# Kernel optimization log

Hardware: AMD Instinct MI355X
Metric: run time of the kernel (lower is better)

## Reference

```python
import jax, jax.numpy as jnp
import numpy as np
from jax.scipy.linalg import expm, solve_triangular

B, N, K, A, V = 2, 256, 16, 16, 32000
ALPHA = 1.0
LAMBDA_BELIEF = 1.0
EPS = 1e-8   # kl_divergence jitter
EPS2 = 1e-6  # pairwise-KL jitter


def _spd(key, b, n, k, scale=0.3):
    a = jax.random.normal(key, (b, n, k, k)) * scale
    return jnp.einsum('bnkl,bnml->bnkm', a, a) + jnp.eye(k)


def setup_inputs() -> dict:
    key = jax.random.key(0)
    ks = jax.random.split(key, 9)
    mu = jax.random.normal(ks[0], (B, N, K))
    Sigma = _spd(ks[1], B, N, K)
    phi = jax.random.normal(ks[2], (B, N, A)) * 0.05
    mu_prior = jax.random.normal(ks[3], (B, N, K))
    Sigma_prior = _spd(ks[4], B, N, K)
    beta = jax.random.uniform(ks[5], (B, N, N)) / N
    W_out = jax.random.normal(ks[6], (V, K)) * 0.02
    R = jax.random.normal(ks[7], (A, K, K))
    generators = (R - jnp.swapaxes(R, -1, -2)) * 0.1  # skew-symmetric Lie generators
    targets = jax.random.randint(ks[8], (B, N), 0, V)
    return {"mu": mu, "Sigma": Sigma, "phi": phi, "mu_prior": mu_prior,
            "Sigma_prior": Sigma_prior, "beta": beta, "W_out": W_out,
            "generators": generators, "targets": targets}


def _bexpm(M):
    # batched matrix exponential over leading dims
    shape = M.shape
    return jax.vmap(expm)(M.reshape(-1, shape[-2], shape[-1])).reshape(shape)


def _potential(mu, Sigma, phi, mu_prior, Sigma_prior, beta, W_out, generators, targets):
    I = jnp.eye(K, dtype=mu.dtype)

    # --- V_self: alpha * sum_n KL(q_n || p_n), explicit-inverse formulation ---
    Sq = Sigma + EPS * I
    Sp = Sigma_prior + EPS * I
    Sp_inv = jnp.linalg.inv(Sp)
    trace_t = jnp.einsum('bnij,bnji->bn', Sp_inv, Sq)
    dmu = mu_prior - mu
    mahal = jnp.einsum('bni,bnij,bnj->bn', dmu, Sp_inv, dmu)
    logdet = jnp.linalg.slogdet(Sp)[1] - jnp.linalg.slogdet(Sq)[1]
    kl_self = 0.5 * (trace_t + mahal - K + logdet)
    V_self = ALPHA * kl_self.sum(-1)

    # --- V_align: pairwise KL under Lie transport Omega_ij = e^{phi_i G} e^{-phi_j G} ---
    phi_mat = jnp.einsum('bna,aij->bnij', phi, generators)          # (B,N,K,K)
    exp_phi = _bexpm(phi_mat)
    exp_neg_phi = _bexpm(-phi_mat)
    Omega = jnp.einsum('bikl,bjlm->bijkm', exp_phi, exp_neg_phi)    # (B,N,N,K,K)
    mu_t = jnp.einsum('bijkl,bjl->bijk', Omega, mu)                 # (B,N,N,K)
    # Omega Sigma_j Omega^T (congruence -> SPD)
    Sigma_t = jnp.einsum('bijkl,bjlm,bijnm->bijkn', Omega, Sigma, Omega)

    Stp = Sigma_t + EPS2 * I
    L_p = jnp.linalg.cholesky(Stp)                                  # (B,N,N,K,K)
    Sigma_i = jnp.broadcast_to((Sigma + EPS2 * I)[:, :, None], (B, N, N, K, K))
    Y = solve_triangular(L_p, Sigma_i, lower=True)
    Z = solve_triangular(jnp.swapaxes(L_p, -1, -2), Y, lower=False)
    trace_term = jnp.diagonal(Z, axis1=-2, axis2=-1).sum(-1)        # (B,N,N)

    delta = mu_t - mu[:, :, None, :]
    v = solve_triangular(L_p, delta[..., None], lower=True)[..., 0]
    mahal_term = (v ** 2).sum(-1)

    logdet_p = 2.0 * jnp.log(jnp.diagonal(L_p, axis1=-2, axis2=-1) + EPS2).sum(-1)
    L_q = jnp.linalg.cholesky(Sigma + EPS2 * I)                     # (B,N,K,K)
    logdet_q = 2.0 * jnp.log(jnp.diagonal(L_q, axis1=-2, axis2=-1) + EPS2).sum(-1)

    kl_all = 0.5 * (trace_term + mahal_term - K + logdet_p - logdet_q[:, :, None])
    kl_all = jnp.maximum(kl_all, 0.0)
    kl_all = kl_all * (1.0 - jnp.eye(N, dtype=mu.dtype))            # zero diagonal
    V_align = LAMBDA_BELIEF * (beta * kl_all).sum((-2, -1))

    # --- V_ce: cross entropy over W_out projection of mu ---
    logits = jnp.einsum('bnk,vk->bnv', mu, W_out)
    logp = jax.nn.log_softmax(logits, axis=-1)
    ce = -jnp.take_along_axis(logp, targets[..., None], axis=-1)[..., 0]
    V_ce = ce.sum(-1)

    return V_self + V_align + V_ce


def reference(mu, Sigma, phi, mu_prior, Sigma_prior, beta, W_out, generators, targets):
    return _potential(mu, Sigma, phi, mu_prior, Sigma_prior, beta, W_out, generators, targets)
```

## Files before the change

kernel.cpp:

```cpp
#include <hip/hip_runtime.h>
#include <math.h>

#define NB 2
#define NN 256
#define KD 16
#define VV 32000
#define EPS_SELF 1e-8f
#define EPS_AL   1e-6f
#define NNODES (NB*NN)

#define CE_ROWS 8
#define CE_CH   32
#define CE_CHUNK (VV/CE_CH)

#define OFF_MT  0
#define OFF_SH  (NNODES*16)
#define OFF_P   (OFF_SH + NNODES*256)
#define OFF_LD  (OFF_P + NNODES*256)
#define OFF_KLS (OFF_LD + NNODES)
#define OFF_CE  (OFF_KLS + NNODES)
#define OFF_AP  (OFF_CE + NNODES)
#define OFF_CEP (OFF_AP + NNODES)
#define WS_FLOATS (OFF_CEP + NNODES*CE_CH)

__device__ inline float blockReduceSum256(float v, float* red) {
  #pragma unroll
  for (int o = 32; o; o >>= 1) v += __shfl_down(v, o);
  __syncthreads();
  if ((threadIdx.x & 63) == 0) red[threadIdx.x >> 6] = v;
  __syncthreads();
  float s = red[0] + red[1] + red[2] + red[3];
  __syncthreads();
  return s;
}

__global__ __launch_bounds__(256) void prep_kernel(
    const float* __restrict__ mu, const float* __restrict__ Sigma,
    const float* __restrict__ phi, const float* __restrict__ mu_prior,
    const float* __restrict__ Sigma_prior, const float* __restrict__ gen,
    float* __restrict__ ws)
{
  __shared__ float bufA[256], bufT[256], bufU[256], bufS[256];
  __shared__ float srow[16], scol[16], vec_s[16], phi_s[16], red[4];
  const int tid = threadIdx.x;
  const int r = tid >> 4, c = tid & 15;
  const int bid = blockIdx.x;
  const int role = bid & 1, node = bid >> 1;

  if (role == 0) {
    if (tid < 16) phi_s[tid] = phi[node*16 + tid];
    bufS[tid] = Sigma[node*256 + tid];
    __syncthreads();
    float pm = 0.f;
    #pragma unroll
    for (int a = 0; a < 16; ++a) pm = fmaf(phi_s[a], gen[a*256 + tid], pm);
    bufA[tid] = pm * 0.125f;
    __syncthreads();
    float Mrow[16];
    #pragma unroll
    for (int j = 0; j < 16; ++j) Mrow[j] = bufA[r*16 + j];
    bufT[tid] = ((r == c) ? 1.f : 0.f) + bufA[tid] * 0.125f;
    __syncthreads();
    for (int k = 7; k >= 1; --k) {
      float acc = 0.f;
      #pragma unroll
      for (int j = 0; j < 16; ++j) acc = fmaf(Mrow[j], bufT[j*16 + c], acc);
      __syncthreads();
      bufT[tid] = ((r == c) ? 1.f : 0.f) + acc / (float)k;
      __syncthreads();
    }
    for (int s = 0; s < 3; ++s) {
      float acc = 0.f;
      #pragma unroll
      for (int j = 0; j < 16; ++j) acc = fmaf(bufT[r*16 + j], bufT[j*16 + c], acc);
      __syncthreads();
      bufT[tid] = acc;
      __syncthreads();
    }
    {
      float acc = 0.f;
      #pragma unroll
      for (int j = 0; j < 16; ++j) acc = fmaf(bufS[r*16 + j], bufT[j*16 + c], acc);
      bufU[tid] = acc;
    }
    __syncthreads();
    {
      float sh = 0.f;
      #pragma unroll
      for (int j = 0; j < 16; ++j) sh = fmaf(bufT[j*16 + r], bufU[j*16 + c], sh);
      sh += (r == c) ? EPS_AL : 0.f;
      ws[OFF_SH + node*256 + tid] = sh;
      bufA[tid] = sh;
    }
    if (tid < 16) vec_s[tid] = mu[node*16 + tid];
    __syncthreads();
    if (tid < 16) {
      float acc = 0.f;
      #pragma unroll
      for (int rr = 0; rr < 16; ++rr) acc = fmaf(bufT[rr*16 + tid], vec_s[rr], acc);
      ws[OFF_MT + node*16 + tid] = acc;
    }
    for (int k = 0; k < 16; ++k) {
      if (r == k) srow[c] = bufA[k*16 + c];
      if (c == k) scol[r] = bufA[r*16 + k];
      __syncthreads();
      float d = srow[k], dinv = 1.f / d;
      float v;
      if (r == k)      v = (c == k) ? dinv : srow[c] * dinv;
      else if (c == k) v = -scol[r] * dinv;
      else             v = fmaf(-scol[r] * dinv, srow[c], bufA[tid]);
      bufA[tid] = v;
      __syncthreads();
    }
    ws[OFF_P + node*256 + tid] = bufA[tid];
  } else {
    bufS[tid] = Sigma[node*256 + tid];
    bufA[tid] = Sigma_prior[node*256 + tid] + ((r == c) ? EPS_SELF : 0.f);
    if (tid < 16) vec_s[tid] = mu_prior[node*16 + tid] - mu[node*16 + tid];
    __syncthreads();
    float ldSp = 0.f;
    for (int k = 0; k < 16; ++k) {
      if (r == k) srow[c] = bufA[k*16 + c];
      if (c == k) scol[r] = bufA[r*16 + k];
      __syncthreads();
      float d = srow[k], dinv = 1.f / d;
      ldSp += logf(d);
      float v;
      if (r == k)      v = (c == k) ? dinv : srow[c] * dinv;
      else if (c == k) v = -scol[r] * dinv;
      else             v = fmaf(-scol[r] * dinv, srow[c], bufA[tid]);
      bufA[tid] = v;
      __syncthreads();
    }
    float sq = bufS[tid] + ((r == c) ? EPS_SELF : 0.f);
    float val = bufA[tid] * (sq + vec_s[r] * vec_s[c]);
    float tot = blockReduceSum256(val, red);
    bufU[tid] = bufS[tid] + ((r == c) ? EPS_SELF : 0.f);
    __syncthreads();
    float ldSq = 0.f;
    for (int k = 0; k < 16; ++k) {
      float d = bufU[k*17];
      ldSq += logf(d);
      if (r > k && c > k) {
        float dinv = 1.f / d;
        bufU[tid] = fmaf(-bufU[r*16 + k] * dinv, bufU[k*16 + c], bufU[tid]);
      }
      __syncthreads();
    }
    bufU[tid] = bufS[tid] + ((r == c) ? EPS_AL : 0.f);
    __syncthreads();
    float ldq = 0.f;
    for (int k = 0; k < 16; ++k) {
      float d = bufU[k*17];
      ldq += 2.f * logf(sqrtf(d) + EPS_AL);
      if (r > k && c > k) {
        float dinv = 1.f / d;
        bufU[tid] = fmaf(-bufU[r*16 + k] * dinv, bufU[k*16 + c], bufU[tid]);
      }
      __syncthreads();
    }
    if (tid == 0) {
      ws[OFF_KLS + node] = 0.5f * (tot - 16.f + ldSp - ldSq);
      ws[OFF_LD + node] = ldq;
    }
  }
}

#define PSTR 257
__global__ __launch_bounds__(256) void align_kernel(
    const float* __restrict__ beta, const float* __restrict__ wsc, float* __restrict__ ws)
{
  __shared__ float ShI[16*PSTR], PJ[16*PSTR];
  __shared__ float mtI[256], mtJ[256], ldI[16], ldJ[16], red[4];
  const int tid = threadIdx.x;
  const int ti = tid & 15, tj = tid >> 4;
  const int bx = blockIdx.x, by = blockIdx.y, bz = blockIdx.z;
  const int nodeI0 = bz*256 + by*16, nodeJ0 = bz*256 + bx*16;

  for (int idx = tid; idx < 16*256; idx += 256) {
    int row = idx >> 8, col = idx & 255;
    ShI[row*PSTR + col] = wsc[OFF_SH + (nodeI0 + row)*256 + col];
    PJ [row*PSTR + col] = wsc[OFF_P  + (nodeJ0 + row)*256 + col];
  }
  mtI[tid] = wsc[OFF_MT + nodeI0*16 + tid];
  mtJ[tid] = wsc[OFF_MT + nodeJ0*16 + tid];
  if (tid < 16) { ldI[tid] = wsc[OFF_LD + nodeI0 + tid]; ldJ[tid] = wsc[OFF_LD + nodeJ0 + tid]; }
  __syncthreads();

  const float* si = &ShI[ti*PSTR];
  const float* pj = &PJ[tj*PSTR];
  float tr = 0.f;
  #pragma unroll 8
  for (int t = 0; t < 256; ++t) tr = fmaf(si[t], pj[t], tr);

  float d[16];
  #pragma unroll
  for (int k = 0; k < 16; ++k) d[k] = mtJ[tj*16+k] - mtI[ti*16+k];
  float mah = 0.f;
  #pragma unroll
  for (int k = 0; k < 16; ++k) {
    float acc = 0.f;
    #pragma unroll
    for (int l = 0; l < 16; ++l) acc = fmaf(pj[k*16+l], d[l], acc);
    mah = fmaf(d[k], acc, mah);
  }

  float kl = 0.5f * (tr + mah - 16.f + ldJ[tj] - ldI[ti]);
  kl = fmaxf(kl, 0.f);
  int gi = by*16 + ti, gj = bx*16 + tj;
  float contrib = (gi == gj) ? 0.f : kl * beta[bz*65536 + gi*256 + gj];
  float tot = blockReduceSum256(contrib, red);
  if (tid == 0) ws[OFF_AP + (bz*16 + by)*16 + bx] = tot;
}

#define DOT16(q0,q1,q2,q3,A) \
  fmaf(q0.x,A[0],fmaf(q0.y,A[1],fmaf(q0.z,A[2],fmaf(q0.w,A[3], \
  fmaf(q1.x,A[4],fmaf(q1.y,A[5],fmaf(q1.z,A[6],fmaf(q1.w,A[7], \
  fmaf(q2.x,A[8],fmaf(q2.y,A[9],fmaf(q2.z,A[10],fmaf(q2.w,A[11], \
  fmaf(q3.x,A[12],fmaf(q3.y,A[13],fmaf(q3.z,A[14],q3.w*A[15])))))))))))))))

__global__ __launch_bounds__(256) void ce1_kernel(
    const float* __restrict__ mu, const float* __restrict__ W,
    float* __restrict__ ws)
{
  __shared__ float mu_s[CE_ROWS*16];
  __shared__ float sred[CE_ROWS*256];
  const int tid = threadIdx.x;
  const int grp = blockIdx.x;
  const int ch  = blockIdx.y;
  const int row0 = grp * CE_ROWS;

  if (tid < CE_ROWS*16) mu_s[tid] = mu[row0*16 + tid];
  __syncthreads();

  float A[CE_ROWS][16];
  #pragma unroll
  for (int r = 0; r < CE_ROWS; ++r)
    #pragma unroll
    for (int k = 0; k < 16; ++k) A[r][k] = mu_s[r*16+k];

  float acc[CE_ROWS];
  #pragma unroll
  for (int r = 0; r < CE_ROWS; ++r) acc[r] = 0.f;

  const float4* W4 = (const float4*)W;
  const int v0 = ch * CE_CHUNK;
  for (int v = v0 + tid; v < v0 + CE_CHUNK; v += 256) {
    float4 q0 = W4[v*4+0], q1 = W4[v*4+1], q2 = W4[v*4+2], q3 = W4[v*4+3];
    #pragma unroll
    for (int r = 0; r < CE_ROWS; ++r) {
      float l = DOT16(q0,q1,q2,q3,A[r]);
      acc[r] += __expf(l);
    }
  }

  #pragma unroll
  for (int r = 0; r < CE_ROWS; ++r) sred[r*256 + tid] = acc[r];
  __syncthreads();
  for (int h = 128; h > 0; h >>= 1) {
    if (tid < h) {
      #pragma unroll
      for (int r = 0; r < CE_ROWS; ++r) sred[r*256+tid] += sred[r*256+tid+h];
    }
    __syncthreads();
  }
  if (tid < CE_ROWS) ws[OFF_CEP + (row0 + tid)*CE_CH + ch] = sred[tid*256];
}

__global__ __launch_bounds__(256) void final_kernel(
    const float* __restrict__ mu, const float* __restrict__ W,
    const int* __restrict__ targets, const float* __restrict__ ws,
    float* __restrict__ out)
{
  __shared__ double red[256];
  const int tid = threadIdx.x;
  double v[2];
  #pragma unroll
  for (int b = 0; b < 2; ++b) {
    int row = b*256 + tid;
    float s = 0.f;
    #pragma unroll
    for (int c2 = 0; c2 < CE_CH; ++c2) s += ws[OFF_CEP + row*CE_CH + c2];
    int t = targets[row];
    float dt = 0.f;
    #pragma unroll
    for (int k = 0; k < 16; ++k) dt = fmaf(mu[row*16+k], W[t*16+k], dt);
    double ce = (double)logf(s) - (double)dt;
    v[b] = (double)ws[OFF_KLS + row] + (double)ws[OFF_AP + row] + ce;
  }
  for (int b = 0; b < 2; ++b) {
    red[tid] = v[b];
    __syncthreads();
    for (int h = 128; h > 0; h >>= 1) {
      if (tid < h) red[tid] += red[tid + h];
      __syncthreads();
    }
    if (tid == 0) out[b] = (float)red[0];
    __syncthreads();
  }
}

extern "C" void kernel_launch(void* const* d_in, const int* in_sizes, int n_in,
                              void* d_out, int out_size, void* d_ws, size_t ws_size,
                              hipStream_t stream) {
  const float* mu          = (const float*)d_in[0];
  const float* Sigma       = (const float*)d_in[1];
  const float* phi         = (const float*)d_in[2];
  const float* mu_prior    = (const float*)d_in[3];
  const float* Sigma_prior = (const float*)d_in[4];
  const float* beta        = (const float*)d_in[5];
  const float* W_out       = (const float*)d_in[6];
  const float* gen         = (const float*)d_in[7];
  const int*   targets     = (const int*)d_in[8];
  float* out = (float*)d_out;
  float* ws  = (float*)d_ws;
  if (ws_size < (size_t)WS_FLOATS * sizeof(float)) return;

  prep_kernel<<<2*NNODES, 256, 0, stream>>>(mu, Sigma, phi, mu_prior, Sigma_prior, gen, ws);
  dim3 ag(16, 16, NB);
  align_kernel<<<ag, 256, 0, stream>>>(beta, ws, ws);
  dim3 cg(NNODES/CE_ROWS, CE_CH);
  ce1_kernel<<<cg, 256, 0, stream>>>(mu, W_out, ws);
  final_kernel<<<1, 256, 0, stream>>>(mu, W_out, targets, ws, out);
}
```

Measured before the change: 54.11 us.

## Rework prep kernel to one wavefront per node with shuffle-based elimination

The prep kernel now handles one node role per 64-lane wavefront instead of one per 256-thread block. Each lane holds four matrix entries in registers and runs the Gauss-Jordan and elimination steps with wave shuffles, using only wave-local LDS waits instead of block-wide barriers. The align kernel's trace loop is vectorised with float4 LDS reads and a padded stride, and the final reduction is split across one block per batch. The aim is to remove the heavy __syncthreads latency in the small serial matrix steps. In exchange there is more register pressure, and the code relies on the wave-local LDS wait being enough for ordering within a wavefront.

```diff
diff --git a/kernel.cpp b/kernel.cpp
--- a/kernel.cpp
+++ b/kernel.cpp
@@ -23,15 +23,59 @@
 #define OFF_CEP (OFF_AP + NNODES)
 #define WS_FLOATS (OFF_CEP + NNODES*CE_CH)
 
-__device__ inline float blockReduceSum256(float v, float* red) {
-  #pragma unroll
-  for (int o = 32; o; o >>= 1) v += __shfl_down(v, o);
-  __syncthreads();
-  if ((threadIdx.x & 63) == 0) red[threadIdx.x >> 6] = v;
-  __syncthreads();
-  float s = red[0] + red[1] + red[2] + red[3];
-  __syncthreads();
-  return s;
+#define WAVE_SYNC() asm volatile("s_waitcnt lgkmcnt(0)" ::: "memory")
+
+__device__ __forceinline__ void ld4(float* dst, const float4 v) {
+  dst[0] = v.x; dst[1] = v.y; dst[2] = v.z; dst[3] = v.w;
+}
+
+__device__ __forceinline__ float dot16a(const float* a, const float* b) {
+  float acc = 0.f;
+  #pragma unroll
+  for (int j = 0; j < 16; ++j) acc = fmaf(a[j], b[j], acc);
+  return acc;
+}
+
+__device__ __forceinline__ void gj16(float aq[4], const int g, const int c, float* ldacc) {
+  #pragma unroll
+  for (int k = 0; k < 16; ++k) {
+    float d    = __shfl(aq[k & 3], ((k >> 2) << 4) | k);
+    float rowk = __shfl(aq[k & 3], ((k >> 2) << 4) | c);
+    float ck[4];
+    #pragma unroll
+    for (int q = 0; q < 4; ++q) ck[q] = __shfl(aq[q], (g << 4) | k);
+    if (ldacc) *ldacc += logf(d);
+    float dinv = 1.f / d;
+    #pragma unroll
+    for (int q = 0; q < 4; ++q) {
+      int r = 4*g + q;
+      float vgen = fmaf(-ck[q] * dinv, rowk, aq[q]);
+      aq[q] = (r == k) ? ((c == k) ? dinv : aq[q] * dinv)
+                       : ((c == k) ? (-ck[q] * dinv) : vgen);
+    }
+  }
+}
+
+template<int QUIRK>
+__device__ __forceinline__ float ge16_logdet(float aq[4], const int g, const int c) {
+  float ld = 0.f;
+  #pragma unroll
+  for (int k = 0; k < 16; ++k) {
+    float d    = __shfl(aq[k & 3], ((k >> 2) << 4) | k);
+    float rowk = __shfl(aq[k & 3], ((k >> 2) << 4) | c);
+    float ck[4];
+    #pragma unroll
+    for (int q = 0; q < 4; ++q) ck[q] = __shfl(aq[q], (g << 4) | k);
+    ld += QUIRK ? 2.f * logf(sqrtf(d) + EPS_AL) : logf(d);
+    float dinv = 1.f / d;
+    #pragma unroll
+    for (int q = 0; q < 4; ++q) {
+      int r = 4*g + q;
+      float upd = fmaf(-ck[q] * dinv, rowk, aq[q]);
+      aq[q] = (r > k && c > k) ? upd : aq[q];
+    }
+  }
+  return ld;
 }
 
 __global__ __launch_bounds__(256) void prep_kernel(
@@ -40,137 +84,186 @@
     const float* __restrict__ Sigma_prior, const float* __restrict__ gen,
     float* __restrict__ ws)
 {
-  __shared__ float bufA[256], bufT[256], bufU[256], bufS[256];
-  __shared__ float srow[16], scol[16], vec_s[16], phi_s[16], red[4];
+  __shared__ __align__(16) float wl[4][980];
   const int tid = threadIdx.x;
-  const int r = tid >> 4, c = tid & 15;
-  const int bid = blockIdx.x;
-  const int role = bid & 1, node = bid >> 1;
+  const int w = tid >> 6, l = tid & 63;
+  const int g = l >> 4, c = l & 15;
+  const int unit = blockIdx.x * 4 + w;
+  const int role = unit & 1, node = unit >> 1;
+  float* COLp = &wl[w][0];
+  float* ROWp = &wl[w][320];
+  float* AUXp = &wl[w][640];
 
   if (role == 0) {
-    if (tid < 16) phi_s[tid] = phi[node*16 + tid];
-    bufS[tid] = Sigma[node*256 + tid];
-    __syncthreads();
-    float pm = 0.f;
-    #pragma unroll
-    for (int a = 0; a < 16; ++a) pm = fmaf(phi_s[a], gen[a*256 + tid], pm);
-    bufA[tid] = pm * 0.125f;
-    __syncthreads();
-    float Mrow[16];
-    #pragma unroll
-    for (int j = 0; j < 16; ++j) Mrow[j] = bufA[r*16 + j];
-    bufT[tid] = ((r == c) ? 1.f : 0.f) + bufA[tid] * 0.125f;
-    __syncthreads();
+    float phis[16];
+    {
+      const float4* p4 = (const float4*)(phi + node*16);
+      ld4(phis, p4[0]); ld4(phis+4, p4[1]); ld4(phis+8, p4[2]); ld4(phis+12, p4[3]);
+    }
+    float x[4] = {0.f, 0.f, 0.f, 0.f};
+    #pragma unroll
+    for (int aa = 0; aa < 16; ++aa) {
+      float4 gq = *(const float4*)(gen + aa*256 + c*16 + 4*g);
+      x[0] = fmaf(phis[aa], gq.x, x[0]);
+      x[1] = fmaf(phis[aa], gq.y, x[1]);
+      x[2] = fmaf(phis[aa], gq.z, x[2]);
+      x[3] = fmaf(phis[aa], gq.w, x[3]);
+    }
+    #pragma unroll
+    for (int q = 0; q < 4; ++q) x[q] *= -0.125f;
+
+    #pragma unroll
+    for (int q = 0; q < 4; ++q) ROWp[(4*g+q)*20 + c] = x[q];
+    WAVE_SYNC();
+    float Mrow[4][16];
+    #pragma unroll
+    for (int q = 0; q < 4; ++q)
+      #pragma unroll
+      for (int j4 = 0; j4 < 4; ++j4)
+        ld4(&Mrow[q][4*j4], *(const float4*)&ROWp[(4*g+q)*20 + 4*j4]);
+
+    float t[4];
+    #pragma unroll
+    for (int q = 0; q < 4; ++q) t[q] = ((4*g+q) == c ? 1.f : 0.f) + x[q]*0.125f;
     for (int k = 7; k >= 1; --k) {
-      float acc = 0.f;
-      #pragma unroll
-      for (int j = 0; j < 16; ++j) acc = fmaf(Mrow[j], bufT[j*16 + c], acc);
-      __syncthreads();
-      bufT[tid] = ((r == c) ? 1.f : 0.f) + acc / (float)k;
-      __syncthreads();
+      *(float4*)&COLp[c*20 + 4*g] = make_float4(t[0], t[1], t[2], t[3]);
+      WAVE_SYNC();
+      float T[16];
+      #pragma unroll
+      for (int j4 = 0; j4 < 4; ++j4) ld4(&T[4*j4], *(const float4*)&COLp[c*20 + 4*j4]);
+      #pragma unroll
+      for (int q = 0; q < 4; ++q)
+        t[q] = ((4*g+q) == c ? 1.f : 0.f) + dot16a(Mrow[q], T) / (float)k;
     }
     for (int s = 0; s < 3; ++s) {
-      float acc = 0.f;
-      #pragma unroll
-      for (int j = 0; j < 16; ++j) acc = fmaf(bufT[r*16 + j], bufT[j*16 + c], acc);
-      __syncthreads();
-      bufT[tid] = acc;
-      __syncthreads();
-    }
-    {
-      float acc = 0.f;
-      #pragma unroll
-      for (int j = 0; j < 16; ++j) acc = fmaf(bufS[r*16 + j], bufT[j*16 + c], acc);
-      bufU[tid] = acc;
-    }
-    __syncthreads();
-    {
-      float sh = 0.f;
-      #pragma unroll
-      for (int j = 0; j < 16; ++j) sh = fmaf(bufT[j*16 + r], bufU[j*16 + c], sh);
-      sh += (r == c) ? EPS_AL : 0.f;
-      ws[OFF_SH + node*256 + tid] = sh;
-      bufA[tid] = sh;
-    }
-    if (tid < 16) vec_s[tid] = mu[node*16 + tid];
-    __syncthreads();
-    if (tid < 16) {
-      float acc = 0.f;
-      #pragma unroll
-      for (int rr = 0; rr < 16; ++rr) acc = fmaf(bufT[rr*16 + tid], vec_s[rr], acc);
-      ws[OFF_MT + node*16 + tid] = acc;
-    }
-    for (int k = 0; k < 16; ++k) {
-      if (r == k) srow[c] = bufA[k*16 + c];
-      if (c == k) scol[r] = bufA[r*16 + k];
-      __syncthreads();
-      float d = srow[k], dinv = 1.f / d;
-      float v;
-      if (r == k)      v = (c == k) ? dinv : srow[c] * dinv;
-      else if (c == k) v = -scol[r] * dinv;
-      else             v = fmaf(-scol[r] * dinv, srow[c], bufA[tid]);
-      bufA[tid] = v;
-      __syncthreads();
-    }
-    ws[OFF_P + node*256 + tid] = bufA[tid];
+      *(float4*)&COLp[c*20 + 4*g] = make_float4(t[0], t[1], t[2], t[3]);
+      #pragma unroll
+      for (int q = 0; q < 4; ++q) ROWp[(4*g+q)*20 + c] = t[q];
+      WAVE_SYNC();
+      float T[16];
+      #pragma unroll
+      for (int j4 = 0; j4 < 4; ++j4) ld4(&T[4*j4], *(const float4*)&COLp[c*20 + 4*j4]);
+      float nt[4];
+      #pragma unroll
+      for (int q = 0; q < 4; ++q) {
+        float acc = 0.f;
+        #pragma unroll
+        for (int j4 = 0; j4 < 4; ++j4) {
+          float4 rv = *(const float4*)&ROWp[(4*g+q)*20 + 4*j4];
+          acc = fmaf(rv.x, T[4*j4+0], acc);
+          acc = fmaf(rv.y, T[4*j4+1], acc);
+          acc = fmaf(rv.z, T[4*j4+2], acc);
+          acc = fmaf(rv.w, T[4*j4+3], acc);
+        }
+        nt[q] = acc;
+      }
+      #pragma unroll
+      for (int q = 0; q < 4; ++q) t[q] = nt[q];
+    }
+    *(float4*)&COLp[c*20 + 4*g] = make_float4(t[0], t[1], t[2], t[3]);
+    WAVE_SYNC();
+    float Ecol[16];
+    #pragma unroll
+    for (int j4 = 0; j4 < 4; ++j4) ld4(&Ecol[4*j4], *(const float4*)&COLp[c*20 + 4*j4]);
+
+    float w1q[4];
+    #pragma unroll
+    for (int q = 0; q < 4; ++q) {
+      float S[16];
+      const float4* s4 = (const float4*)(Sigma + node*256 + (4*g+q)*16);
+      ld4(S, s4[0]); ld4(S+4, s4[1]); ld4(S+8, s4[2]); ld4(S+12, s4[3]);
+      w1q[q] = dot16a(S, Ecol);
+    }
+    *(float4*)&AUXp[c*20 + 4*g] = make_float4(w1q[0], w1q[1], w1q[2], w1q[3]);
+    WAVE_SYNC();
+    float W1c[16];
+    #pragma unroll
+    for (int j4 = 0; j4 < 4; ++j4) ld4(&W1c[4*j4], *(const float4*)&AUXp[c*20 + 4*j4]);
+
+    float sh[4];
+    #pragma unroll
+    for (int q = 0; q < 4; ++q) {
+      float Er[16];
+      #pragma unroll
+      for (int j4 = 0; j4 < 4; ++j4) ld4(&Er[4*j4], *(const float4*)&COLp[(4*g+q)*20 + 4*j4]);
+      sh[q] = dot16a(Er, W1c) + ((4*g+q) == c ? EPS_AL : 0.f);
+    }
+    *(float4*)(ws + OFF_SH + node*256 + c*16 + 4*g) = make_float4(sh[0], sh[1], sh[2], sh[3]);
+
+    {
+      float muv[16];
+      const float4* m4 = (const float4*)(mu + node*16);
+      ld4(muv, m4[0]); ld4(muv+4, m4[1]); ld4(muv+8, m4[2]); ld4(muv+12, m4[3]);
+      float mt = dot16a(Ecol, muv);
+      if (g == 0) ws[OFF_MT + node*16 + c] = mt;
+    }
+    gj16(sh, g, c, (float*)nullptr);
+    *(float4*)(ws + OFF_P + node*256 + c*16 + 4*g) = make_float4(sh[0], sh[1], sh[2], sh[3]);
   } else {
-    bufS[tid] = Sigma[node*256 + tid];
-    bufA[tid] = Sigma_prior[node*256 + tid] + ((r == c) ? EPS_SELF : 0.f);
-    if (tid < 16) vec_s[tid] = mu_prior[node*16 + tid] - mu[node*16 + tid];
-    __syncthreads();
+    float sp[4];
+    {
+      float4 v = *(const float4*)(Sigma_prior + node*256 + c*16 + 4*g);
+      sp[0] = v.x + ((4*g+0 == c) ? EPS_SELF : 0.f);
+      sp[1] = v.y + ((4*g+1 == c) ? EPS_SELF : 0.f);
+      sp[2] = v.z + ((4*g+2 == c) ? EPS_SELF : 0.f);
+      sp[3] = v.w + ((4*g+3 == c) ? EPS_SELF : 0.f);
+    }
     float ldSp = 0.f;
-    for (int k = 0; k < 16; ++k) {
-      if (r == k) srow[c] = bufA[k*16 + c];
-      if (c == k) scol[r] = bufA[r*16 + k];
-      __syncthreads();
-      float d = srow[k], dinv = 1.f / d;
-      ldSp += logf(d);
-      float v;
-      if (r == k)      v = (c == k) ? dinv : srow[c] * dinv;
-      else if (c == k) v = -scol[r] * dinv;
-      else             v = fmaf(-scol[r] * dinv, srow[c], bufA[tid]);
-      bufA[tid] = v;
-      __syncthreads();
-    }
-    float sq = bufS[tid] + ((r == c) ? EPS_SELF : 0.f);
-    float val = bufA[tid] * (sq + vec_s[r] * vec_s[c]);
-    float tot = blockReduceSum256(val, red);
-    bufU[tid] = bufS[tid] + ((r == c) ? EPS_SELF : 0.f);
-    __syncthreads();
-    float ldSq = 0.f;
-    for (int k = 0; k < 16; ++k) {
-      float d = bufU[k*17];
-      ldSq += logf(d);
-      if (r > k && c > k) {
-        float dinv = 1.f / d;
-        bufU[tid] = fmaf(-bufU[r*16 + k] * dinv, bufU[k*16 + c], bufU[tid]);
-      }
-      __syncthreads();
-    }
-    bufU[tid] = bufS[tid] + ((r == c) ? EPS_AL : 0.f);
-    __syncthreads();
-    float ldq = 0.f;
-    for (int k = 0; k < 16; ++k) {
-      float d = bufU[k*17];
-      ldq += 2.f * logf(sqrtf(d) + EPS_AL);
-      if (r > k && c > k) {
-        float dinv = 1.f / d;
-        bufU[tid] = fmaf(-bufU[r*16 + k] * dinv, bufU[k*16 + c], bufU[tid]);
-      }
-      __syncthreads();
-    }
-    if (tid == 0) {
-      ws[OFF_KLS + node] = 0.5f * (tot - 16.f + ldSp - ldSq);
-      ws[OFF_LD + node] = ldq;
-    }
-  }
-}
-
-#define PSTR 257
+    gj16(sp, g, c, &ldSp);
+
+    float dmur[4], dmuc;
+    {
+      float4 a = *(const float4*)(mu_prior + node*16 + 4*g);
+      float4 b = *(const float4*)(mu + node*16 + 4*g);
+      dmur[0] = a.x - b.x; dmur[1] = a.y - b.y; dmur[2] = a.z - b.z; dmur[3] = a.w - b.w;
+      dmuc = mu_prior[node*16 + c] - mu[node*16 + c];
+    }
+    float val = 0.f;
+    {
+      float4 v = *(const float4*)(Sigma + node*256 + c*16 + 4*g);
+      float s0 = v.x + ((4*g+0 == c) ? EPS_SELF : 0.f);
+      float s1 = v.y + ((4*g+1 == c) ? EPS_SELF : 0.f);
+      float s2 = v.z + ((4*g+2 == c) ? EPS_SELF : 0.f);
+      float s3 = v.w + ((4*g+3 == c) ? EPS_SELF : 0.f);
+      val = fmaf(sp[0], s0 + dmur[0]*dmuc, val);
+      val = fmaf(sp[1], s1 + dmur[1]*dmuc, val);
+      val = fmaf(sp[2], s2 + dmur[2]*dmuc, val);
+      val = fmaf(sp[3], s3 + dmur[3]*dmuc, val);
+    }
+    #pragma unroll
+    for (int o = 32; o; o >>= 1) val += __shfl_xor(val, o);
+
+    float sq[4];
+    {
+      float4 v = *(const float4*)(Sigma + node*256 + c*16 + 4*g);
+      sq[0] = v.x + ((4*g+0 == c) ? EPS_SELF : 0.f);
+      sq[1] = v.y + ((4*g+1 == c) ? EPS_SELF : 0.f);
+      sq[2] = v.z + ((4*g+2 == c) ? EPS_SELF : 0.f);
+      sq[3] = v.w + ((4*g+3 == c) ? EPS_SELF : 0.f);
+    }
+    float ldSq = ge16_logdet<0>(sq, g, c);
+    float sg[4];
+    {
+      float4 v = *(const float4*)(Sigma + node*256 + c*16 + 4*g);
+      sg[0] = v.x + ((4*g+0 == c) ? EPS_AL : 0.f);
+      sg[1] = v.y + ((4*g+1 == c) ? EPS_AL : 0.f);
+      sg[2] = v.z + ((4*g+2 == c) ? EPS_AL : 0.f);
+      sg[3] = v.w + ((4*g+3 == c) ? EPS_AL : 0.f);
+    }
+    float ldq = ge16_logdet<1>(sg, g, c);
+    if (l == 0) {
+      ws[OFF_KLS + node] = 0.5f * (val - 16.f + ldSp - ldSq);
+      ws[OFF_LD + node]  = ldq;
+    }
+  }
+}
+
+#define PSTR 260
 __global__ __launch_bounds__(256) void align_kernel(
     const float* __restrict__ beta, const float* __restrict__ wsc, float* __restrict__ ws)
 {
-  __shared__ float ShI[16*PSTR], PJ[16*PSTR];
+  __shared__ __align__(16) float ShI[16*PSTR];
+  __shared__ __align__(16) float PJ[16*PSTR];
   __shared__ float mtI[256], mtJ[256], ldI[16], ldJ[16], red[4];
   const int tid = threadIdx.x;
   const int ti = tid & 15, tj = tid >> 4;
@@ -187,12 +280,19 @@
   if (tid < 16) { ldI[tid] = wsc[OFF_LD + nodeI0 + tid]; ldJ[tid] = wsc[OFF_LD + nodeJ0 + tid]; }
   __syncthreads();
 
-  const float* si = &ShI[ti*PSTR];
+  const float4* si4 = (const float4*)&ShI[ti*PSTR];
+  const float4* pj4 = (const float4*)&PJ[tj*PSTR];
+  float tr = 0.f;
+  #pragma unroll 16
+  for (int t = 0; t < 64; ++t) {
+    float4 xv = si4[t], yv = pj4[t];
+    tr = fmaf(xv.x, yv.x, tr);
+    tr = fmaf(xv.y, yv.y, tr);
+    tr = fmaf(xv.z, yv.z, tr);
+    tr = fmaf(xv.w, yv.w, tr);
+  }
+
   const float* pj = &PJ[tj*PSTR];
-  float tr = 0.f;
-  #pragma unroll 8
-  for (int t = 0; t < 256; ++t) tr = fmaf(si[t], pj[t], tr);
-
   float d[16];
   #pragma unroll
   for (int k = 0; k < 16; ++k) d[k] = mtJ[tj*16+k] - mtI[ti*16+k];
@@ -201,7 +301,7 @@
   for (int k = 0; k < 16; ++k) {
     float acc = 0.f;
     #pragma unroll
-    for (int l = 0; l < 16; ++l) acc = fmaf(pj[k*16+l], d[l], acc);
+    for (int ll = 0; ll < 16; ++ll) acc = fmaf(pj[k*16+ll], d[ll], acc);
     mah = fmaf(d[k], acc, mah);
   }
 
@@ -209,8 +309,12 @@
   kl = fmaxf(kl, 0.f);
   int gi = by*16 + ti, gj = bx*16 + tj;
   float contrib = (gi == gj) ? 0.f : kl * beta[bz*65536 + gi*256 + gj];
-  float tot = blockReduceSum256(contrib, red);
-  if (tid == 0) ws[OFF_AP + (bz*16 + by)*16 + bx] = tot;
+  #pragma unroll
+  for (int o = 32; o; o >>= 1) contrib += __shfl_down(contrib, o);
+  __syncthreads();
+  if ((tid & 63) == 0) red[tid >> 6] = contrib;
+  __syncthreads();
+  if (tid == 0) ws[OFF_AP + (bz*16 + by)*16 + bx] = red[0] + red[1] + red[2] + red[3];
 }
 
 #define DOT16(q0,q1,q2,q3,A) \
@@ -249,8 +353,8 @@
     float4 q0 = W4[v*4+0], q1 = W4[v*4+1], q2 = W4[v*4+2], q3 = W4[v*4+3];
     #pragma unroll
     for (int r = 0; r < CE_ROWS; ++r) {
-      float l = DOT16(q0,q1,q2,q3,A[r]);
-      acc[r] += __expf(l);
+      float lg = DOT16(q0,q1,q2,q3,A[r]);
+      acc[r] += __expf(lg);
     }
   }
 
@@ -274,30 +378,23 @@
 {
   __shared__ double red[256];
   const int tid = threadIdx.x;
-  double v[2];
-  #pragma unroll
-  for (int b = 0; b < 2; ++b) {
-    int row = b*256 + tid;
-    float s = 0.f;
-    #pragma unroll
-    for (int c2 = 0; c2 < CE_CH; ++c2) s += ws[OFF_CEP + row*CE_CH + c2];
-    int t = targets[row];
-    float dt = 0.f;
-    #pragma unroll
-    for (int k = 0; k < 16; ++k) dt = fmaf(mu[row*16+k], W[t*16+k], dt);
-    double ce = (double)logf(s) - (double)dt;
-    v[b] = (double)ws[OFF_KLS + row] + (double)ws[OFF_AP + row] + ce;
-  }
-  for (int b = 0; b < 2; ++b) {
-    red[tid] = v[b];
+  const int b = blockIdx.x;
+  const int row = b*256 + tid;
+  float s = 0.f;
+  #pragma unroll
+  for (int c2 = 0; c2 < CE_CH; ++c2) s += ws[OFF_CEP + row*CE_CH + c2];
+  int t = targets[row];
+  float dt = 0.f;
+  #pragma unroll
+  for (int k = 0; k < 16; ++k) dt = fmaf(mu[row*16+k], W[t*16+k], dt);
+  double ce = (double)logf(s) - (double)dt;
+  red[tid] = (double)ws[OFF_KLS + row] + (double)ws[OFF_AP + row] + ce;
+  __syncthreads();
+  for (int h = 128; h > 0; h >>= 1) {
+    if (tid < h) red[tid] += red[tid + h];
     __syncthreads();
-    for (int h = 128; h > 0; h >>= 1) {
-      if (tid < h) red[tid] += red[tid + h];
-      __syncthreads();
-    }
-    if (tid == 0) out[b] = (float)red[0];
-    __syncthreads();
-  }
+  }
+  if (tid == 0) out[b] = (float)red[0];
 }
 
 extern "C" void kernel_launch(void* const* d_in, const int* in_sizes, int n_in,
@@ -316,10 +413,10 @@
   float* ws  = (float*)d_ws;
   if (ws_size < (size_t)WS_FLOATS * sizeof(float)) return;
 
-  prep_kernel<<<2*NNODES, 256, 0, stream>>>(mu, Sigma, phi, mu_prior, Sigma_prior, gen, ws);
+  prep_kernel<<<256, 256, 0, stream>>>(mu, Sigma, phi, mu_prior, Sigma_prior, gen, ws);
   dim3 ag(16, 16, NB);
   align_kernel<<<ag, 256, 0, stream>>>(beta, ws, ws);
   dim3 cg(NNODES/CE_ROWS, CE_CH);
   ce1_kernel<<<cg, 256, 0, stream>>>(mu, W_out, ws);
-  final_kernel<<<1, 256, 0, stream>>>(mu, W_out, targets, ws, out);
-}
+  final_kernel<<<NB, 256, 0, stream>>>(mu, W_out, targets, ws, out);
+}
```

After: 43.36 us. 19.9% less time.
